# Kernel tuning notes

Measured on AMD Instinct MI355X. Metric: run time of the kernel, lower is better.

The kernel has to match this reference:

```python
import jax, jax.numpy as jnp
import numpy as np

EPS = 1e-5
POOL = 4  # two stacked AvgPool3d(2) == one AvgPool3d(4, stride=4) on the valid region


def setup_inputs() -> dict:
    key = jax.random.key(0)
    k1, k2, k3 = jax.random.split(key, 3)
    N, Cin, Cout, D = 16, 32, 16, 32
    x = jax.random.normal(k1, (N, Cin, D, D, D), dtype=jnp.float32)
    w = jax.random.normal(k2, (Cin, Cout, 3, 3, 3), dtype=jnp.float32) * 0.1
    b = jax.random.normal(k3, (Cout,), dtype=jnp.float32) * 0.1
    gamma = jnp.ones((Cout,), dtype=jnp.float32)
    beta = jnp.zeros((Cout,), dtype=jnp.float32)
    return {"x": x, "w": w, "b": b, "gamma": gamma, "beta": beta}


def _convT_bn_pool(x, w, b, gamma, beta):
    # ConvTranspose3d(stride=2, padding=1, K=3) == dilated conv with
    # lhs_dilation=2, padding=K-1-p=1, spatially-flipped kernel, IO->OI swap.
    wt = jnp.flip(w, axis=(2, 3, 4)).transpose(1, 0, 2, 3, 4)  # [Cout,Cin,3,3,3]
    y = jax.lax.conv_general_dilated(
        x, wt,
        window_strides=(1, 1, 1),
        padding=[(1, 1), (1, 1), (1, 1)],
        lhs_dilation=(2, 2, 2),
        dimension_numbers=("NCDHW", "OIDHW", "NCDHW"),
    )
    y = y + b[None, :, None, None, None]  # [N,Cout,Dout,Hout,Wout], Dout=2D-1

    # BatchNorm training stats: biased variance over (N,D,H,W) per channel
    mean = jnp.mean(y, axis=(0, 2, 3, 4), keepdims=True)
    var = jnp.mean(jnp.square(y - mean), axis=(0, 2, 3, 4), keepdims=True)
    inv = jax.lax.rsqrt(var + EPS)
    yn = (y - mean) * inv * gamma[None, :, None, None, None] + beta[None, :, None, None, None]

    # Two AvgPool3d(2) == AvgPool3d(4, stride 4) on the cropped valid region
    N_, C_, Do, Ho, Wo = yn.shape
    D2, H2, W2 = Do // POOL, Ho // POOL, Wo // POOL
    yn = yn[:, :, : D2 * POOL, : H2 * POOL, : W2 * POOL]
    yn = yn.reshape(N_, C_, D2, POOL, H2, POOL, W2, POOL)
    return jnp.mean(yn, axis=(3, 5, 7))  # [N,C,D2,H2,W2]


def reference(x, w, b, gamma, beta):
    return _convT_bn_pool(x, w, b, gamma, beta)
```

## Files before the change

kernel.cpp:

```cpp
#include <hip/hip_runtime.h>


typedef __attribute__((ext_vector_type(8))) short bf16x8;
typedef __attribute__((ext_vector_type(4))) float f32x4;

static __device__ __forceinline__ unsigned short f2bf(float f) {
    unsigned int u = __float_as_uint(f);
    u = (u + 0x7fffu + ((u >> 16) & 1u)) >> 16;
    return (unsigned short)u;
}

__global__ __launch_bounds__(256)
void kw(const float* __restrict__ w, unsigned short* __restrict__ wT)
{
    const int idx = blockIdx.x * 256 + threadIdx.x;
    if (idx < 13824) {
        const int ci = idx & 31, co = (idx >> 5) & 15, tap = idx >> 9;
        wT[idx] = f2bf(w[(ci * 16 + co) * 27 + tap]);
    }
}

__global__ __launch_bounds__(256, 3)
void convf(const float* __restrict__ x,
           const unsigned short* __restrict__ wT,
           const float* __restrict__ bias,
           float* __restrict__ pooled,
           float* __restrict__ psum, float* __restrict__ psq)
{
    const int ht = blockIdx.x, dt = blockIdx.y, n = blockIdx.z;
    const int tid = threadIdx.x;
    const int v = tid >> 6, lane = tid & 63;
    const int t = v & 1, odp = v >> 1;
    const int c = lane & 15, qd = lane >> 4;
    const int m = c;

    __shared__ unsigned short xs[9504];
    __shared__ unsigned short wsm[13824];
    __shared__ float sred[4][16], qred[4][16], pbuf[2][8][16];

    const int id0 = dt * 2, ih0 = ht * 2;

    if (tid < 144) {
        const int dihi = tid >> 4, kk = tid & 15;
        ((unsigned int*)xs)[((dihi * 1056 + 1024) >> 1) + kk] = 0u;
    }
    for (int it = 0; it < 9; ++it) {
        const int idx = tid + 256 * it;
        const int row = idx >> 3, seg = idx & 7;
        const int ci = row / 9, dihi = row - ci * 9;
        const int di = dihi / 3, hi = dihi - di * 3;
        const int id = id0 + di, ih = ih0 + hi;
        float4 val = make_float4(0.f, 0.f, 0.f, 0.f);
        if (id < 32 && ih < 32)
            val = *(const float4*)(x + ((((n*32 + ci)*32 + id)*32 + ih)*32) + seg*4);
        const int g = (ci >> 3) ^ (seg & 3);
        const int base = dihi * 1056 + (seg * 4) * 32 + g * 8 + (ci & 7);
        xs[base +  0] = f2bf(val.x);
        xs[base + 32] = f2bf(val.y);
        xs[base + 64] = f2bf(val.z);
        xs[base + 96] = f2bf(val.w);
    }
    for (int i = tid; i < 1728; i += 256)
        ((uint4*)wsm)[i] = ((const uint4*)wT)[i];
    __syncthreads();

    f32x4 acc[2][4][2];
    #pragma unroll
    for (int ol = 0; ol < 2; ++ol)
        #pragma unroll
        for (int oh = 0; oh < 4; ++oh)
            #pragma unroll
            for (int par = 0; par < 2; ++par)
                acc[ol][oh][par] = (f32x4){0.f, 0.f, 0.f, 0.f};

    auto LDA = [&](int di, int hi, int sofs) -> bf16x8 {
        const int iw = 16 * t + sofs + m;
        const int g  = qd ^ ((iw >> 2) & 3);
        return *(const bf16x8*)(xs + (di*3 + hi) * 1056 + iw * 32 + g * 8);
    };
    auto LDB = [&](int tap) -> bf16x8 {
        return *(const bf16x8*)(wsm + tap * 512 + c * 32 + qd * 8);
    };

    constexpr int HN[3] = {2, 3, 1};
    constexpr int HKH[3][3] = {{1,2,0},{0,1,2},{0,0,0}};
    constexpr int HOH[3][3] = {{0,1,0},{1,2,3},{3,0,0}};

    bf16x8 A0[3], A1[3];
    #pragma unroll
    for (int hi = 0; hi < 3; ++hi) { A0[hi] = LDA(odp, hi, 0); A1[hi] = LDA(odp, hi, 1); }

    #pragma unroll
    for (int kdi = 0; kdi < 2; ++kdi) {
        const int kd = kdi + 1, ol = kdi;
        bf16x8 Bf[3][3];
        #pragma unroll
        for (int kh = 0; kh < 3; ++kh)
            #pragma unroll
            for (int kw2 = 0; kw2 < 3; ++kw2)
                Bf[kh][kw2] = LDB(kd*9 + kh*3 + kw2);
        #pragma unroll
        for (int hi = 0; hi < 3; ++hi)
            #pragma unroll
            for (int j = 0; j < 3; ++j)
                if (j < HN[hi]) {
                    const int kh = HKH[hi][j], oh = HOH[hi][j];
                    acc[ol][oh][0] = __builtin_amdgcn_mfma_f32_16x16x32_bf16(
                        A0[hi], Bf[kh][1], acc[ol][oh][0], 0, 0, 0);
                    acc[ol][oh][1] = __builtin_amdgcn_mfma_f32_16x16x32_bf16(
                        A1[hi], Bf[kh][0], acc[ol][oh][1], 0, 0, 0);
                    acc[ol][oh][1] = __builtin_amdgcn_mfma_f32_16x16x32_bf16(
                        A0[hi], Bf[kh][2], acc[ol][oh][1], 0, 0, 0);
                }
    }

    #pragma unroll
    for (int hi = 0; hi < 3; ++hi) { A0[hi] = LDA(odp+1, hi, 0); A1[hi] = LDA(odp+1, hi, 1); }
    {
        bf16x8 Bf[3][3];
        #pragma unroll
        for (int kh = 0; kh < 3; ++kh)
            #pragma unroll
            for (int kw2 = 0; kw2 < 3; ++kw2)
                Bf[kh][kw2] = LDB(kh*3 + kw2);
        #pragma unroll
        for (int hi = 0; hi < 3; ++hi)
            #pragma unroll
            for (int j = 0; j < 3; ++j)
                if (j < HN[hi]) {
                    const int kh = HKH[hi][j], oh = HOH[hi][j];
                    acc[1][oh][0] = __builtin_amdgcn_mfma_f32_16x16x32_bf16(
                        A0[hi], Bf[kh][1], acc[1][oh][0], 0, 0, 0);
                    acc[1][oh][1] = __builtin_amdgcn_mfma_f32_16x16x32_bf16(
                        A1[hi], Bf[kh][0], acc[1][oh][1], 0, 0, 0);
                    acc[1][oh][1] = __builtin_amdgcn_mfma_f32_16x16x32_bf16(
                        A0[hi], Bf[kh][2], acc[1][oh][1], 0, 0, 0);
                }
    }

    const float bv = bias[c];
    float s = 0.f, sq = 0.f;
    float P[2] = {0.f, 0.f};
    #pragma unroll
    for (int ol = 0; ol < 2; ++ol) {
        const int odg = 2*odp + ol;
        const bool odok = !(dt == 15 && odg == 3);
        #pragma unroll
        for (int oh = 0; oh < 4; ++oh) {
            const bool ohok = !(ht == 15 && oh == 3);
            #pragma unroll
            for (int par = 0; par < 2; ++par) {
                #pragma unroll
                for (int r = 0; r < 4; ++r) {
                    const float val = acc[ol][oh][par][r] + bv;
                    const bool owok = !(par == 1 && t == 1 && qd == 3 && r == 3);
                    if (odok && ohok && owok) { s += val; sq += val * val; }
                    P[r >> 1] += val;
                }
            }
        }
    }
    s  += __shfl_xor(s, 16, 64);  s  += __shfl_xor(s, 32, 64);
    sq += __shfl_xor(sq, 16, 64); sq += __shfl_xor(sq, 32, 64);

    if (lane < 16) { sred[v][lane] = s; qred[v][lane] = sq; }
    if (odp == 0 && dt < 15 && ht < 15) {
        pbuf[t][2*qd + 0][c] = P[0];
        pbuf[t][2*qd + 1][c] = P[1];
    }
    __syncthreads();
    if (tid < 16) {
        const int blk = (n*16 + dt)*16 + ht;
        psum[tid*4096 + blk] = sred[0][tid]+sred[1][tid]+sred[2][tid]+sred[3][tid];
        psq [tid*4096 + blk] = qred[0][tid]+qred[1][tid]+qred[2][tid]+qred[3][tid];
    }
    if (odp == 1 && dt < 15 && ht < 15) {
        #pragma unroll
        for (int jj = 0; jj < 2; ++jj) {
            const int jl = 2*qd + jj, jg = 8*t + jl;
            if (jg < 15) {
                const float tot = pbuf[t][jl][c] + P[jj];
                pooled[(n*16 + c)*3375 + dt*225 + ht*15 + jg] = tot * (1.f/64.f);
            }
        }
    }
}

__global__ void bnfinal(const float* __restrict__ psum, const float* __restrict__ psq,
                        const float* __restrict__ gamma, const float* __restrict__ beta,
                        float* __restrict__ bn)
{
    const int co = blockIdx.x;
    const int t  = threadIdx.x;
    float S = 0, Q = 0;
    for (int blk = t; blk < 4096; blk += 256) {
        S += psum[co*4096 + blk];
        Q += psq [co*4096 + blk];
    }
    #pragma unroll
    for (int off = 32; off > 0; off >>= 1) {
        S += __shfl_down(S, off, 64);
        Q += __shfl_down(Q, off, 64);
    }
    __shared__ float rs[4], rq[4];
    if ((t & 63) == 0) { rs[t >> 6] = S; rq[t >> 6] = Q; }
    __syncthreads();
    if (t == 0) {
        S = rs[0] + rs[1] + rs[2] + rs[3];
        Q = rq[0] + rq[1] + rq[2] + rq[3];
        const float cnt = 16.f * 63.f * 63.f * 63.f;
        const float mean = S / cnt;
        const float var  = Q / cnt - mean * mean;
        const float inv  = rsqrtf(var + 1e-5f);
        const float sc   = inv * gamma[co];
        bn[co]      = sc;
        bn[16 + co] = beta[co] - mean * sc;
    }
}

__global__ void finalize(const float* __restrict__ pooled, const float* __restrict__ bn,
                         float* __restrict__ out)
{
    const int i  = blockIdx.x * 256 + threadIdx.x;
    const int co = (i / 3375) & 15;
    out[i] = pooled[i] * bn[co] + bn[16 + co];
}

extern "C" void kernel_launch(void* const* d_in, const int* in_sizes, int n_in,
                              void* d_out, int out_size, void* d_ws, size_t ws_size,
                              hipStream_t stream)
{
    const float* x     = (const float*)d_in[0];
    const float* w     = (const float*)d_in[1];
    const float* b     = (const float*)d_in[2];
    const float* gamma = (const float*)d_in[3];
    const float* beta  = (const float*)d_in[4];
    float* out = (float*)d_out;

    char* wsb = (char*)d_ws;
    unsigned short* wT = (unsigned short*)wsb;
    float* pooled = (float*)(wsb + 27648);
    float* psum   = (float*)(wsb + 27648 + 3456000);
    float* psq    = (float*)(wsb + 27648 + 3456000 + 262144);
    float* bn     = (float*)(wsb + 27648 + 3456000 + 2*262144);

    kw<<<54, 256, 0, stream>>>(w, wT);
    dim3 grid(16, 16, 16);
    convf<<<grid, 256, 0, stream>>>(x, wT, b, pooled, psum, psq);
    bnfinal<<<16, 256, 0, stream>>>(psum, psq, gamma, beta, bn);
    finalize<<<3375, 256, 0, stream>>>(pooled, bn, out);
}
```

Measured before the change: 150.9 us.

## Fuse all stages into one persistent kernel with grid barrier and depth loop

Replaces the four-kernel pipeline with a single persistent kernel of 256 blocks. Each block loops over all depth tiles for one (n, h-tile) pair and keeps a rolling 3-slot LDS ring of input planes, so overlapping depth planes are reused and global loads are prefetched in registers. The 27 weight fragments are held in registers across the loop. BatchNorm statistics are reduced with global atomics and a spin-wait grid barrier, and pooled values stay in LDS until the final normalized write. This removes the extra launches and the global round trip for the pooled and partial-sum buffers. In exchange the grid drops from 4096 blocks to 256 at one block per CU, which lowers parallelism and latency hiding, and the barrier assumes all 256 blocks are resident at once.

```diff
diff --git a/kernel.cpp b/kernel.cpp
--- a/kernel.cpp
+++ b/kernel.cpp
@@ -9,221 +9,250 @@
     u = (u + 0x7fffu + ((u >> 16) & 1u)) >> 16;
     return (unsigned short)u;
 }
-
-__global__ __launch_bounds__(256)
-void kw(const float* __restrict__ w, unsigned short* __restrict__ wT)
+static __device__ __forceinline__ unsigned pack2(float a, float b) {
+    return (unsigned)f2bf(a) | ((unsigned)f2bf(b) << 16);
+}
+
+__global__ __launch_bounds__(256, 1)
+void mega(const float* __restrict__ x, const float* __restrict__ w,
+          const float* __restrict__ bias, const float* __restrict__ gamma,
+          const float* __restrict__ beta, float* __restrict__ out,
+          float* __restrict__ gsum, float* __restrict__ gsq,
+          unsigned int* __restrict__ bar)
 {
-    const int idx = blockIdx.x * 256 + threadIdx.x;
-    if (idx < 13824) {
-        const int ci = idx & 31, co = (idx >> 5) & 15, tap = idx >> 9;
-        wT[idx] = f2bf(w[(ci * 16 + co) * 27 + tap]);
-    }
-}
-
-__global__ __launch_bounds__(256, 3)
-void convf(const float* __restrict__ x,
-           const unsigned short* __restrict__ wT,
-           const float* __restrict__ bias,
-           float* __restrict__ pooled,
-           float* __restrict__ psum, float* __restrict__ psq)
-{
-    const int ht = blockIdx.x, dt = blockIdx.y, n = blockIdx.z;
+    const int ht = blockIdx.x & 15, n = blockIdx.x >> 4;
     const int tid = threadIdx.x;
     const int v = tid >> 6, lane = tid & 63;
     const int t = v & 1, odp = v >> 1;
     const int c = lane & 15, qd = lane >> 4;
-    const int m = c;
-
+
+    __shared__ unsigned short wsm[13824];
     __shared__ unsigned short xs[9504];
-    __shared__ unsigned short wsm[13824];
+    __shared__ float plds[3600];
     __shared__ float sred[4][16], qred[4][16], pbuf[2][8][16];
-
-    const int id0 = dt * 2, ih0 = ht * 2;
-
-    if (tid < 144) {
-        const int dihi = tid >> 4, kk = tid & 15;
-        ((unsigned int*)xs)[((dihi * 1056 + 1024) >> 1) + kk] = 0u;
-    }
-    for (int it = 0; it < 9; ++it) {
-        const int idx = tid + 256 * it;
-        const int row = idx >> 3, seg = idx & 7;
-        const int ci = row / 9, dihi = row - ci * 9;
-        const int di = dihi / 3, hi = dihi - di * 3;
-        const int id = id0 + di, ih = ih0 + hi;
-        float4 val = make_float4(0.f, 0.f, 0.f, 0.f);
-        if (id < 32 && ih < 32)
-            val = *(const float4*)(x + ((((n*32 + ci)*32 + id)*32 + ih)*32) + seg*4);
-        const int g = (ci >> 3) ^ (seg & 3);
-        const int base = dihi * 1056 + (seg * 4) * 32 + g * 8 + (ci & 7);
-        xs[base +  0] = f2bf(val.x);
-        xs[base + 32] = f2bf(val.y);
-        xs[base + 64] = f2bf(val.z);
-        xs[base + 96] = f2bf(val.w);
-    }
-    for (int i = tid; i < 1728; i += 256)
-        ((uint4*)wsm)[i] = ((const uint4*)wT)[i];
-    __syncthreads();
-
-    f32x4 acc[2][4][2];
+    __shared__ float bnco[32];
+
+    const int ih0 = ht * 2;
+
+    #pragma unroll 1
+    for (int k = 0; k < 54; ++k) {
+        const int idx = tid + 256 * k;
+        const int ci = idx / 432, r = idx - ci * 432;
+        const int co = r / 27, tap = r - co * 27;
+        wsm[tap * 512 + co * 32 + ci] = f2bf(w[idx]);
+    }
+
+    auto stage_single = [&](int id) {
+        const int slot = id % 3;
+        #pragma unroll
+        for (int r = 0; r < 2; ++r) {
+            const int combo = r * 16 + (tid >> 4);
+            if (combo >= 24) continue;
+            const int seg = combo & 7, ihl = combo >> 3;
+            const int ih = ih0 + ihl;
+            const int cp = tid & 15, ci0 = cp * 2;
+            f32x4 a = {0.f,0.f,0.f,0.f}, b = {0.f,0.f,0.f,0.f};
+            if (id < 32 && ih < 32) {
+                const float* px = x + (((n*32 + ci0)*32 + id)*32 + ih)*32 + seg*4;
+                a = *(const f32x4*)px;
+                b = *(const f32x4*)(px + 32768);
+            }
+            const int base = slot * 3168 + ihl * 1056;
+            #pragma unroll
+            for (int j = 0; j < 4; ++j) {
+                const int iw = seg * 4 + j;
+                const int g = (cp >> 2) ^ ((iw >> 2) & 3);
+                *(unsigned*)(xs + base + iw*32 + g*8 + 2*(cp & 3)) = pack2(a[j], b[j]);
+            }
+            if (seg == 7)
+                *(unsigned*)(xs + base + 1024 + (cp >> 2)*8 + 2*(cp & 3)) = 0u;
+        }
+    };
+
+    f32x4 F[6];
+    auto prefetch = [&](int idA) {
+        #pragma unroll
+        for (int r = 0; r < 3; ++r) {
+            const int combo = r * 16 + (tid >> 4);
+            const int seg = combo & 7, q = combo >> 3;
+            const int p = (q >= 3) ? 1 : 0, ihl = q - 3 * p;
+            const int id = idA + p, ih = ih0 + ihl;
+            const int ci0 = (tid & 15) * 2;
+            f32x4 z = {0.f,0.f,0.f,0.f};
+            F[2*r] = z; F[2*r+1] = z;
+            if (id < 32 && ih < 32) {
+                const float* px = x + (((n*32 + ci0)*32 + id)*32 + ih)*32 + seg*4;
+                F[2*r]   = *(const f32x4*)px;
+                F[2*r+1] = *(const f32x4*)(px + 32768);
+            }
+        }
+    };
+    auto writebatch = [&](int idA) {
+        #pragma unroll
+        for (int r = 0; r < 3; ++r) {
+            const int combo = r * 16 + (tid >> 4);
+            const int seg = combo & 7, q = combo >> 3;
+            const int p = (q >= 3) ? 1 : 0, ihl = q - 3 * p;
+            const int id = idA + p;
+            const int slot = id % 3;
+            const int cp = tid & 15;
+            const int base = slot * 3168 + ihl * 1056;
+            #pragma unroll
+            for (int j = 0; j < 4; ++j) {
+                const int iw = seg * 4 + j;
+                const int g = (cp >> 2) ^ ((iw >> 2) & 3);
+                *(unsigned*)(xs + base + iw*32 + g*8 + 2*(cp & 3)) =
+                    pack2(F[2*r][j], F[2*r+1][j]);
+            }
+            if (seg == 7)
+                *(unsigned*)(xs + base + 1024 + (cp >> 2)*8 + 2*(cp & 3)) = 0u;
+        }
+    };
+
+    stage_single(0); stage_single(1); stage_single(2);
+    prefetch(3);
+
+    __syncthreads();
+
+    bf16x8 Bfr[27];
     #pragma unroll
-    for (int ol = 0; ol < 2; ++ol)
-        #pragma unroll
-        for (int oh = 0; oh < 4; ++oh)
-            #pragma unroll
-            for (int par = 0; par < 2; ++par)
-                acc[ol][oh][par] = (f32x4){0.f, 0.f, 0.f, 0.f};
-
-    auto LDA = [&](int di, int hi, int sofs) -> bf16x8 {
-        const int iw = 16 * t + sofs + m;
-        const int g  = qd ^ ((iw >> 2) & 3);
-        return *(const bf16x8*)(xs + (di*3 + hi) * 1056 + iw * 32 + g * 8);
-    };
-    auto LDB = [&](int tap) -> bf16x8 {
-        return *(const bf16x8*)(wsm + tap * 512 + c * 32 + qd * 8);
-    };
+    for (int tap = 0; tap < 27; ++tap)
+        Bfr[tap] = *(const bf16x8*)(wsm + tap * 512 + c * 32 + qd * 8);
 
     constexpr int HN[3] = {2, 3, 1};
     constexpr int HKH[3][3] = {{1,2,0},{0,1,2},{0,0,0}};
     constexpr int HOH[3][3] = {{0,1,0},{1,2,3},{3,0,0}};
 
-    bf16x8 A0[3], A1[3];
-    #pragma unroll
-    for (int hi = 0; hi < 3; ++hi) { A0[hi] = LDA(odp, hi, 0); A1[hi] = LDA(odp, hi, 1); }
-
-    #pragma unroll
-    for (int kdi = 0; kdi < 2; ++kdi) {
-        const int kd = kdi + 1, ol = kdi;
-        bf16x8 Bf[3][3];
-        #pragma unroll
-        for (int kh = 0; kh < 3; ++kh)
-            #pragma unroll
-            for (int kw2 = 0; kw2 < 3; ++kw2)
-                Bf[kh][kw2] = LDB(kd*9 + kh*3 + kw2);
+    const float bv = bias[c];
+    float s = 0.f, sq = 0.f;
+
+    for (int dt = 0; dt < 16; ++dt) {
+        const int b0 = ((2*dt + odp)     % 3) * 3168;
+        const int b1 = ((2*dt + odp + 1) % 3) * 3168;
+        auto LDA = [&](int base, int hi, int sofs) -> bf16x8 {
+            const int iw = 16*t + sofs + c;
+            const int g  = qd ^ ((iw >> 2) & 3);
+            return *(const bf16x8*)(xs + base + hi*1056 + iw*32 + g*8);
+        };
+        bf16x8 A0[3], A1[3], C0[3], C1[3];
+        #pragma unroll
+        for (int hi = 0; hi < 3; ++hi) {
+            A0[hi] = LDA(b0, hi, 0); A1[hi] = LDA(b0, hi, 1);
+            C0[hi] = LDA(b1, hi, 0); C1[hi] = LDA(b1, hi, 1);
+        }
+        f32x4 acc[2][4][2];
+        #pragma unroll
+        for (int ol = 0; ol < 2; ++ol)
+            #pragma unroll
+            for (int oh = 0; oh < 4; ++oh)
+                #pragma unroll
+                for (int par = 0; par < 2; ++par)
+                    acc[ol][oh][par] = (f32x4){0.f,0.f,0.f,0.f};
+
         #pragma unroll
         for (int hi = 0; hi < 3; ++hi)
             #pragma unroll
             for (int j = 0; j < 3; ++j)
                 if (j < HN[hi]) {
                     const int kh = HKH[hi][j], oh = HOH[hi][j];
-                    acc[ol][oh][0] = __builtin_amdgcn_mfma_f32_16x16x32_bf16(
-                        A0[hi], Bf[kh][1], acc[ol][oh][0], 0, 0, 0);
-                    acc[ol][oh][1] = __builtin_amdgcn_mfma_f32_16x16x32_bf16(
-                        A1[hi], Bf[kh][0], acc[ol][oh][1], 0, 0, 0);
-                    acc[ol][oh][1] = __builtin_amdgcn_mfma_f32_16x16x32_bf16(
-                        A0[hi], Bf[kh][2], acc[ol][oh][1], 0, 0, 0);
+                    acc[0][oh][0] = __builtin_amdgcn_mfma_f32_16x16x32_bf16(
+                        A0[hi], Bfr[9 + kh*3 + 1], acc[0][oh][0], 0, 0, 0);
+                    acc[0][oh][1] = __builtin_amdgcn_mfma_f32_16x16x32_bf16(
+                        A1[hi], Bfr[9 + kh*3 + 0], acc[0][oh][1], 0, 0, 0);
+                    acc[0][oh][1] = __builtin_amdgcn_mfma_f32_16x16x32_bf16(
+                        A0[hi], Bfr[9 + kh*3 + 2], acc[0][oh][1], 0, 0, 0);
+                    acc[1][oh][0] = __builtin_amdgcn_mfma_f32_16x16x32_bf16(
+                        A0[hi], Bfr[18 + kh*3 + 1], acc[1][oh][0], 0, 0, 0);
+                    acc[1][oh][1] = __builtin_amdgcn_mfma_f32_16x16x32_bf16(
+                        A1[hi], Bfr[18 + kh*3 + 0], acc[1][oh][1], 0, 0, 0);
+                    acc[1][oh][1] = __builtin_amdgcn_mfma_f32_16x16x32_bf16(
+                        A0[hi], Bfr[18 + kh*3 + 2], acc[1][oh][1], 0, 0, 0);
+                    acc[1][oh][0] = __builtin_amdgcn_mfma_f32_16x16x32_bf16(
+                        C0[hi], Bfr[kh*3 + 1], acc[1][oh][0], 0, 0, 0);
+                    acc[1][oh][1] = __builtin_amdgcn_mfma_f32_16x16x32_bf16(
+                        C1[hi], Bfr[kh*3 + 0], acc[1][oh][1], 0, 0, 0);
+                    acc[1][oh][1] = __builtin_amdgcn_mfma_f32_16x16x32_bf16(
+                        C0[hi], Bfr[kh*3 + 2], acc[1][oh][1], 0, 0, 0);
                 }
-    }
-
-    #pragma unroll
-    for (int hi = 0; hi < 3; ++hi) { A0[hi] = LDA(odp+1, hi, 0); A1[hi] = LDA(odp+1, hi, 1); }
-    {
-        bf16x8 Bf[3][3];
-        #pragma unroll
-        for (int kh = 0; kh < 3; ++kh)
-            #pragma unroll
-            for (int kw2 = 0; kw2 < 3; ++kw2)
-                Bf[kh][kw2] = LDB(kh*3 + kw2);
-        #pragma unroll
-        for (int hi = 0; hi < 3; ++hi)
-            #pragma unroll
-            for (int j = 0; j < 3; ++j)
-                if (j < HN[hi]) {
-                    const int kh = HKH[hi][j], oh = HOH[hi][j];
-                    acc[1][oh][0] = __builtin_amdgcn_mfma_f32_16x16x32_bf16(
-                        A0[hi], Bf[kh][1], acc[1][oh][0], 0, 0, 0);
-                    acc[1][oh][1] = __builtin_amdgcn_mfma_f32_16x16x32_bf16(
-                        A1[hi], Bf[kh][0], acc[1][oh][1], 0, 0, 0);
-                    acc[1][oh][1] = __builtin_amdgcn_mfma_f32_16x16x32_bf16(
-                        A0[hi], Bf[kh][2], acc[1][oh][1], 0, 0, 0);
-                }
-    }
-
-    const float bv = bias[c];
-    float s = 0.f, sq = 0.f;
-    float P[2] = {0.f, 0.f};
-    #pragma unroll
-    for (int ol = 0; ol < 2; ++ol) {
-        const int odg = 2*odp + ol;
-        const bool odok = !(dt == 15 && odg == 3);
-        #pragma unroll
-        for (int oh = 0; oh < 4; ++oh) {
-            const bool ohok = !(ht == 15 && oh == 3);
-            #pragma unroll
-            for (int par = 0; par < 2; ++par) {
+
+        float P[2] = {0.f, 0.f};
+        #pragma unroll
+        for (int ol = 0; ol < 2; ++ol) {
+            const bool odok = !(dt == 15 && odp == 1 && ol == 1);
+            #pragma unroll
+            for (int oh = 0; oh < 4; ++oh) {
+                const bool ohok = !(ht == 15 && oh == 3);
                 #pragma unroll
-                for (int r = 0; r < 4; ++r) {
-                    const float val = acc[ol][oh][par][r] + bv;
-                    const bool owok = !(par == 1 && t == 1 && qd == 3 && r == 3);
-                    if (odok && ohok && owok) { s += val; sq += val * val; }
-                    P[r >> 1] += val;
-                }
-            }
-        }
-    }
+                for (int par = 0; par < 2; ++par)
+                    #pragma unroll
+                    for (int r = 0; r < 4; ++r) {
+                        const float val = acc[ol][oh][par][r] + bv;
+                        const bool owok = !(par == 1 && t == 1 && qd == 3 && r == 3);
+                        const float mk = (odok && ohok && owok) ? 1.f : 0.f;
+                        s += mk * val; sq += mk * val * val;
+                        P[r >> 1] += val;
+                    }
+            }
+        }
+        if (odp == 0 && dt < 15 && ht < 15) {
+            pbuf[t][2*qd + 0][c] = P[0];
+            pbuf[t][2*qd + 1][c] = P[1];
+        }
+        __syncthreads();
+        if (odp == 1 && dt < 15 && ht < 15) {
+            #pragma unroll
+            for (int jj = 0; jj < 2; ++jj) {
+                const int jl = 2*qd + jj, jg = 8*t + jl;
+                if (jg < 15)
+                    plds[c*225 + dt*15 + jg] = pbuf[t][jl][c] + P[jj];
+            }
+        }
+        if (dt < 15) {
+            writebatch(2*dt + 3);
+            if (dt < 14) prefetch(2*dt + 5);
+        }
+        __syncthreads();
+    }
+
     s  += __shfl_xor(s, 16, 64);  s  += __shfl_xor(s, 32, 64);
     sq += __shfl_xor(sq, 16, 64); sq += __shfl_xor(sq, 32, 64);
-
     if (lane < 16) { sred[v][lane] = s; qred[v][lane] = sq; }
-    if (odp == 0 && dt < 15 && ht < 15) {
-        pbuf[t][2*qd + 0][c] = P[0];
-        pbuf[t][2*qd + 1][c] = P[1];
-    }
     __syncthreads();
     if (tid < 16) {
-        const int blk = (n*16 + dt)*16 + ht;
-        psum[tid*4096 + blk] = sred[0][tid]+sred[1][tid]+sred[2][tid]+sred[3][tid];
-        psq [tid*4096 + blk] = qred[0][tid]+qred[1][tid]+qred[2][tid]+qred[3][tid];
-    }
-    if (odp == 1 && dt < 15 && ht < 15) {
-        #pragma unroll
-        for (int jj = 0; jj < 2; ++jj) {
-            const int jl = 2*qd + jj, jg = 8*t + jl;
-            if (jg < 15) {
-                const float tot = pbuf[t][jl][c] + P[jj];
-                pooled[(n*16 + c)*3375 + dt*225 + ht*15 + jg] = tot * (1.f/64.f);
-            }
-        }
-    }
-}
-
-__global__ void bnfinal(const float* __restrict__ psum, const float* __restrict__ psq,
-                        const float* __restrict__ gamma, const float* __restrict__ beta,
-                        float* __restrict__ bn)
-{
-    const int co = blockIdx.x;
-    const int t  = threadIdx.x;
-    float S = 0, Q = 0;
-    for (int blk = t; blk < 4096; blk += 256) {
-        S += psum[co*4096 + blk];
-        Q += psq [co*4096 + blk];
-    }
-    #pragma unroll
-    for (int off = 32; off > 0; off >>= 1) {
-        S += __shfl_down(S, off, 64);
-        Q += __shfl_down(Q, off, 64);
-    }
-    __shared__ float rs[4], rq[4];
-    if ((t & 63) == 0) { rs[t >> 6] = S; rq[t >> 6] = Q; }
-    __syncthreads();
-    if (t == 0) {
-        S = rs[0] + rs[1] + rs[2] + rs[3];
-        Q = rq[0] + rq[1] + rq[2] + rq[3];
-        const float cnt = 16.f * 63.f * 63.f * 63.f;
+        atomicAdd(&gsum[tid], sred[0][tid]+sred[1][tid]+sred[2][tid]+sred[3][tid]);
+        atomicAdd(&gsq [tid], qred[0][tid]+qred[1][tid]+qred[2][tid]+qred[3][tid]);
+    }
+
+    __syncthreads();
+    if (tid == 0) {
+        __threadfence();
+        atomicAdd(bar, 1u);
+        while (atomicAdd(bar, 0u) < 256u) __builtin_amdgcn_s_sleep(2);
+        __threadfence();
+    }
+    __syncthreads();
+
+    if (tid < 16) {
+        const float S = atomicAdd(&gsum[tid], 0.f);
+        const float Q = atomicAdd(&gsq[tid], 0.f);
+        const float cnt  = 16.f * 63.f * 63.f * 63.f;
         const float mean = S / cnt;
         const float var  = Q / cnt - mean * mean;
         const float inv  = rsqrtf(var + 1e-5f);
-        const float sc   = inv * gamma[co];
-        bn[co]      = sc;
-        bn[16 + co] = beta[co] - mean * sc;
-    }
-}
-
-__global__ void finalize(const float* __restrict__ pooled, const float* __restrict__ bn,
-                         float* __restrict__ out)
-{
-    const int i  = blockIdx.x * 256 + threadIdx.x;
-    const int co = (i / 3375) & 15;
-    out[i] = pooled[i] * bn[co] + bn[16 + co];
+        const float sc   = inv * gamma[tid];
+        bnco[tid]      = sc;
+        bnco[16 + tid] = beta[tid] - mean * sc;
+    }
+    __syncthreads();
+
+    if (ht < 15) {
+        for (int i = tid; i < 3600; i += 256) {
+            const int co = i / 225, rem = i - co * 225;
+            const int dq = rem / 15, wq = rem - dq * 15;
+            out[((n*16 + co)*15 + dq)*225 + ht*15 + wq] =
+                plds[i] * (1.f/64.f) * bnco[co] + bnco[16 + co];
+        }
+    }
 }
 
 extern "C" void kernel_launch(void* const* d_in, const int* in_sizes, int n_in,
@@ -237,16 +266,10 @@
     const float* beta  = (const float*)d_in[4];
     float* out = (float*)d_out;
 
-    char* wsb = (char*)d_ws;
-    unsigned short* wT = (unsigned short*)wsb;
-    float* pooled = (float*)(wsb + 27648);
-    float* psum   = (float*)(wsb + 27648 + 3456000);
-    float* psq    = (float*)(wsb + 27648 + 3456000 + 262144);
-    float* bn     = (float*)(wsb + 27648 + 3456000 + 2*262144);
-
-    kw<<<54, 256, 0, stream>>>(w, wT);
-    dim3 grid(16, 16, 16);
-    convf<<<grid, 256, 0, stream>>>(x, wT, b, pooled, psum, psq);
-    bnfinal<<<16, 256, 0, stream>>>(psum, psq, gamma, beta, bn);
-    finalize<<<3375, 256, 0, stream>>>(pooled, bn, out);
-}
+    float* gsum = (float*)d_ws;
+    float* gsq  = gsum + 16;
+    unsigned int* bar = (unsigned int*)(gsq + 16);
+
+    hipMemsetAsync(d_ws, 0, 256, stream);
+    mega<<<256, 256, 0, stream>>>(x, w, b, gamma, beta, out, gsum, gsq, bar);
+}
```

Result: slower. 156.6 us (+3.8%).

## Drop shared weight staging, reload B fragments from global, repack input tile layout

Applied to the files above, without the earlier changes.

The conv kernel no longer stages the 27 KB bf16 weight table in LDS. Each wave now loads its B fragments straight from global/L2 per kd phase, with the first phase issued before the barrier. The input tile is gathered so each thread packs 8 channels into one 16-byte LDS store, giving a new unswizzled layout with padding, and A fragments are loaded per hi inside the phase. This cuts LDS use, which could raise occupancy, and shrinks the prologue, but it adds redundant global weight reads and uses strided 4-byte global loads for x in place of float4.

```diff
diff --git a/kernel.cpp b/kernel.cpp
--- a/kernel.cpp
+++ b/kernel.cpp
@@ -9,6 +9,9 @@
     u = (u + 0x7fffu + ((u >> 16) & 1u)) >> 16;
     return (unsigned short)u;
 }
+static __device__ __forceinline__ unsigned pack2(float a, float b) {
+    return (unsigned)f2bf(a) | ((unsigned)f2bf(b) << 16);
+}
 
 __global__ __launch_bounds__(256)
 void kw(const float* __restrict__ w, unsigned short* __restrict__ wT)
@@ -21,47 +24,52 @@
 }
 
 __global__ __launch_bounds__(256, 3)
-void convf(const float* __restrict__ x,
-           const unsigned short* __restrict__ wT,
-           const float* __restrict__ bias,
-           float* __restrict__ pooled,
-           float* __restrict__ psum, float* __restrict__ psq)
+void convf2(const float* __restrict__ x,
+            const unsigned short* __restrict__ wT,
+            const float* __restrict__ bias,
+            float* __restrict__ pooled,
+            float* __restrict__ psum, float* __restrict__ psq)
 {
     const int ht = blockIdx.x, dt = blockIdx.y, n = blockIdx.z;
     const int tid = threadIdx.x;
     const int v = tid >> 6, lane = tid & 63;
     const int t = v & 1, odp = v >> 1;
     const int c = lane & 15, qd = lane >> 4;
-    const int m = c;
 
     __shared__ unsigned short xs[9504];
-    __shared__ unsigned short wsm[13824];
     __shared__ float sred[4][16], qred[4][16], pbuf[2][8][16];
 
-    const int id0 = dt * 2, ih0 = ht * 2;
-
-    if (tid < 144) {
-        const int dihi = tid >> 4, kk = tid & 15;
-        ((unsigned int*)xs)[((dihi * 1056 + 1024) >> 1) + kk] = 0u;
-    }
-    for (int it = 0; it < 9; ++it) {
-        const int idx = tid + 256 * it;
-        const int row = idx >> 3, seg = idx & 7;
-        const int ci = row / 9, dihi = row - ci * 9;
-        const int di = dihi / 3, hi = dihi - di * 3;
-        const int id = id0 + di, ih = ih0 + hi;
-        float4 val = make_float4(0.f, 0.f, 0.f, 0.f);
-        if (id < 32 && ih < 32)
-            val = *(const float4*)(x + ((((n*32 + ci)*32 + id)*32 + ih)*32) + seg*4);
-        const int g = (ci >> 3) ^ (seg & 3);
-        const int base = dihi * 1056 + (seg * 4) * 32 + g * 8 + (ci & 7);
-        xs[base +  0] = f2bf(val.x);
-        xs[base + 32] = f2bf(val.y);
-        xs[base + 64] = f2bf(val.z);
-        xs[base + 96] = f2bf(val.w);
-    }
-    for (int i = tid; i < 1728; i += 256)
-        ((uint4*)wsm)[i] = ((const uint4*)wT)[i];
+    #pragma unroll
+    for (int p = 0; p < 5; ++p) {
+        const int dihi = p * 2 + (tid >> 7);
+        if (dihi < 9) {
+            const int iw = tid & 31, g = (tid >> 5) & 3;
+            const int di = dihi / 3, hi = dihi - di * 3;
+            const int id = 2*dt + di, ih = 2*ht + hi;
+            const bool ok = (id < 32) && (ih < 32);
+            const float* px = x + ((((n*32 + g*8)*32 + id)*32 + ih)*32) + iw;
+            float f[8];
+            #pragma unroll
+            for (int j = 0; j < 8; ++j)
+                f[j] = ok ? px[j * 32768] : 0.f;
+            uint4 u;
+            u.x = pack2(f[0], f[1]); u.y = pack2(f[2], f[3]);
+            u.z = pack2(f[4], f[5]); u.w = pack2(f[6], f[7]);
+            *(uint4*)(xs + dihi*1056 + g*264 + iw*8) = u;
+        }
+    }
+    if (tid < 36) {
+        const int dihi = tid >> 2, g = tid & 3;
+        *(uint4*)(xs + dihi*1056 + g*264 + 256) = make_uint4(0,0,0,0);
+    }
+
+    auto LDBg = [&](int tap) -> bf16x8 {
+        return *(const bf16x8*)(wT + tap * 512 + c * 32 + qd * 8);
+    };
+    bf16x8 Ba[9];
+    #pragma unroll
+    for (int i = 0; i < 9; ++i) Ba[i] = LDBg(9 + i);
+
     __syncthreads();
 
     f32x4 acc[2][4][2];
@@ -71,72 +79,42 @@
         for (int oh = 0; oh < 4; ++oh)
             #pragma unroll
             for (int par = 0; par < 2; ++par)
-                acc[ol][oh][par] = (f32x4){0.f, 0.f, 0.f, 0.f};
-
-    auto LDA = [&](int di, int hi, int sofs) -> bf16x8 {
-        const int iw = 16 * t + sofs + m;
-        const int g  = qd ^ ((iw >> 2) & 3);
-        return *(const bf16x8*)(xs + (di*3 + hi) * 1056 + iw * 32 + g * 8);
-    };
-    auto LDB = [&](int tap) -> bf16x8 {
-        return *(const bf16x8*)(wsm + tap * 512 + c * 32 + qd * 8);
+                acc[ol][oh][par] = (f32x4){0.f,0.f,0.f,0.f};
+
+    const int iwb = 16 * t + c;
+    auto LDA = [&](int dihi, int sofs) -> bf16x8 {
+        return *(const bf16x8*)(xs + dihi*1056 + qd*264 + (iwb + sofs)*8);
     };
 
     constexpr int HN[3] = {2, 3, 1};
     constexpr int HKH[3][3] = {{1,2,0},{0,1,2},{0,0,0}};
     constexpr int HOH[3][3] = {{0,1,0},{1,2,3},{3,0,0}};
 
-    bf16x8 A0[3], A1[3];
-    #pragma unroll
-    for (int hi = 0; hi < 3; ++hi) { A0[hi] = LDA(odp, hi, 0); A1[hi] = LDA(odp, hi, 1); }
-
-    #pragma unroll
-    for (int kdi = 0; kdi < 2; ++kdi) {
-        const int kd = kdi + 1, ol = kdi;
-        bf16x8 Bf[3][3];
-        #pragma unroll
-        for (int kh = 0; kh < 3; ++kh)
-            #pragma unroll
-            for (int kw2 = 0; kw2 < 3; ++kw2)
-                Bf[kh][kw2] = LDB(kd*9 + kh*3 + kw2);
-        #pragma unroll
-        for (int hi = 0; hi < 3; ++hi)
+    auto PH = [&](int ol, const bf16x8* B, int di) {
+        #pragma unroll
+        for (int hi = 0; hi < 3; ++hi) {
+            const bf16x8 A0 = LDA(di*3 + hi, 0), A1 = LDA(di*3 + hi, 1);
             #pragma unroll
             for (int j = 0; j < 3; ++j)
                 if (j < HN[hi]) {
                     const int kh = HKH[hi][j], oh = HOH[hi][j];
                     acc[ol][oh][0] = __builtin_amdgcn_mfma_f32_16x16x32_bf16(
-                        A0[hi], Bf[kh][1], acc[ol][oh][0], 0, 0, 0);
+                        A0, B[kh*3 + 1], acc[ol][oh][0], 0, 0, 0);
                     acc[ol][oh][1] = __builtin_amdgcn_mfma_f32_16x16x32_bf16(
-                        A1[hi], Bf[kh][0], acc[ol][oh][1], 0, 0, 0);
+                        A1, B[kh*3 + 0], acc[ol][oh][1], 0, 0, 0);
                     acc[ol][oh][1] = __builtin_amdgcn_mfma_f32_16x16x32_bf16(
-                        A0[hi], Bf[kh][2], acc[ol][oh][1], 0, 0, 0);
+                        A0, B[kh*3 + 2], acc[ol][oh][1], 0, 0, 0);
                 }
-    }
-
-    #pragma unroll
-    for (int hi = 0; hi < 3; ++hi) { A0[hi] = LDA(odp+1, hi, 0); A1[hi] = LDA(odp+1, hi, 1); }
-    {
-        bf16x8 Bf[3][3];
-        #pragma unroll
-        for (int kh = 0; kh < 3; ++kh)
-            #pragma unroll
-            for (int kw2 = 0; kw2 < 3; ++kw2)
-                Bf[kh][kw2] = LDB(kh*3 + kw2);
-        #pragma unroll
-        for (int hi = 0; hi < 3; ++hi)
-            #pragma unroll
-            for (int j = 0; j < 3; ++j)
-                if (j < HN[hi]) {
-                    const int kh = HKH[hi][j], oh = HOH[hi][j];
-                    acc[1][oh][0] = __builtin_amdgcn_mfma_f32_16x16x32_bf16(
-                        A0[hi], Bf[kh][1], acc[1][oh][0], 0, 0, 0);
-                    acc[1][oh][1] = __builtin_amdgcn_mfma_f32_16x16x32_bf16(
-                        A1[hi], Bf[kh][0], acc[1][oh][1], 0, 0, 0);
-                    acc[1][oh][1] = __builtin_amdgcn_mfma_f32_16x16x32_bf16(
-                        A0[hi], Bf[kh][2], acc[1][oh][1], 0, 0, 0);
-                }
-    }
+        }
+    };
+
+    PH(0, Ba, odp);
+    #pragma unroll
+    for (int i = 0; i < 9; ++i) Ba[i] = LDBg(18 + i);
+    PH(1, Ba, odp);
+    #pragma unroll
+    for (int i = 0; i < 9; ++i) Ba[i] = LDBg(i);
+    PH(1, Ba, odp + 1);
 
     const float bv = bias[c];
     float s = 0.f, sq = 0.f;
@@ -149,15 +127,15 @@
         for (int oh = 0; oh < 4; ++oh) {
             const bool ohok = !(ht == 15 && oh == 3);
             #pragma unroll
-            for (int par = 0; par < 2; ++par) {
+            for (int par = 0; par < 2; ++par)
                 #pragma unroll
                 for (int r = 0; r < 4; ++r) {
                     const float val = acc[ol][oh][par][r] + bv;
                     const bool owok = !(par == 1 && t == 1 && qd == 3 && r == 3);
-                    if (odok && ohok && owok) { s += val; sq += val * val; }
+                    const float mk = (odok && ohok && owok) ? 1.f : 0.f;
+                    s += mk * val; sq += mk * val * val;
                     P[r >> 1] += val;
                 }
-            }
         }
     }
     s  += __shfl_xor(s, 16, 64);  s  += __shfl_xor(s, 32, 64);
@@ -246,7 +224,7 @@
 
     kw<<<54, 256, 0, stream>>>(w, wT);
     dim3 grid(16, 16, 16);
-    convf<<<grid, 256, 0, stream>>>(x, wT, b, pooled, psum, psq);
+    convf2<<<grid, 256, 0, stream>>>(x, wT, b, pooled, psum, psq);
     bnfinal<<<16, 256, 0, stream>>>(psum, psq, gamma, beta, bn);
     finalize<<<3375, 256, 0, stream>>>(pooled, bn, out);
 }
```

Result: faster. 144.2 us (-4.4%).
